# Optimization experiments

Measured on AMD Instinct MI355X. Metric: run time of the kernel, lower is better.

## Reference

```python
import jax, jax.numpy as jnp
import numpy as np

B, N, CIN, COUT, R, K = 8, 4096, 64, 128, 32, 3
GROUPS = 8
GN_EPS = 1e-5


def setup_inputs() -> dict:
    key = jax.random.key(0)
    ks = jax.random.split(key, 6)
    w = lambda k, shape, fan: jax.random.normal(k, shape, jnp.float32) / np.sqrt(fan)
    return dict(
        features=jax.random.normal(ks[0], (B, CIN, N), jnp.float32),
        coords=jax.random.uniform(ks[1], (B, N, 3), jnp.float32),
        conv1_w=w(ks[2], (COUT, CIN, K, K, K), CIN * K ** 3), conv1_b=jnp.zeros((COUT,), jnp.float32),
        gn1_g=jnp.ones((COUT,), jnp.float32), gn1_b=jnp.zeros((COUT,), jnp.float32),
        conv2_w=w(ks[3], (COUT, COUT, K, K, K), COUT * K ** 3), conv2_b=jnp.zeros((COUT,), jnp.float32),
        gn2_g=jnp.ones((COUT,), jnp.float32), gn2_b=jnp.zeros((COUT,), jnp.float32),
        pt_w=w(ks[4], (COUT, CIN), CIN), pt_b=jnp.zeros((COUT,), jnp.float32),
        ptgn_g=jnp.ones((COUT,), jnp.float32), ptgn_b=jnp.zeros((COUT,), jnp.float32),
    )


def swish(x):
    return x * jax.nn.sigmoid(x)


def group_norm(x, gamma, beta):
    # x: [B, C, *spatial]
    b, c = x.shape[0], x.shape[1]
    sp = x.shape[2:]
    xg = x.reshape(b, GROUPS, -1)
    m = xg.mean(-1, keepdims=True)
    v = xg.var(-1, keepdims=True)
    xg = (xg - m) * jax.lax.rsqrt(v + GN_EPS)
    x = xg.reshape(b, c, *sp)
    shape = (1, c) + (1,) * len(sp)
    return x * gamma.reshape(shape) + beta.reshape(shape)


def conv3d(x, w, bias):
    p = K // 2
    y = jax.lax.conv_general_dilated(
        x, w, window_strides=(1, 1, 1), padding=[(p, p)] * 3,
        dimension_numbers=('NCDHW', 'OIDHW', 'NCDHW'))
    return y + bias[None, :, None, None, None]


def voxelize(features, coords):
    # PVCNN avg_voxelize: normalize coords to [0, R-1], round, scatter-mean.
    c = coords - coords.mean(axis=1, keepdims=True)          # [B,N,3]
    scale = 2.0 * jnp.linalg.norm(c, axis=-1).max(axis=1)     # [B], eps=0
    norm_coords = c / scale[:, None, None] + 0.5
    norm_coords = jnp.clip(norm_coords * R, 0.0, R - 1)       # float coords in [0, R-1]
    vox = jnp.round(norm_coords).astype(jnp.int32)
    flat = (vox[..., 0] * R + vox[..., 1]) * R + vox[..., 2]  # [B,N]
    seg = (flat + jnp.arange(B, dtype=jnp.int32)[:, None] * R ** 3).reshape(-1)
    ft = features.transpose(0, 2, 1).reshape(B * N, CIN)
    sums = jax.ops.segment_sum(ft, seg, num_segments=B * R ** 3)
    cnt = jax.ops.segment_sum(jnp.ones((B * N,), ft.dtype), seg, num_segments=B * R ** 3)
    grid = sums / jnp.maximum(cnt, 1.0)[:, None]
    grid = grid.reshape(B, R ** 3, CIN).transpose(0, 2, 1).reshape(B, CIN, R, R, R)
    return grid, norm_coords


def trilinear_devoxelize(grid, norm_coords):
    # grid: [B, C, R, R, R]; norm_coords: [B, N, 3] float in [0, R-1]
    c = grid.shape[1]
    f = jnp.floor(norm_coords)
    d = norm_coords - f                                       # frac, [B,N,3]
    f0 = f.astype(jnp.int32)
    f1 = jnp.minimum(f0 + 1, R - 1)
    gridf = grid.reshape(B, c, R ** 3)
    out = jnp.zeros((B, c, N), grid.dtype)
    for ix in (0, 1):
        for iy in (0, 1):
            for iz in (0, 1):
                xi = f1[..., 0] if ix else f0[..., 0]
                yi = f1[..., 1] if iy else f0[..., 1]
                zi = f1[..., 2] if iz else f0[..., 2]
                wx = d[..., 0] if ix else 1.0 - d[..., 0]
                wy = d[..., 1] if iy else 1.0 - d[..., 1]
                wz = d[..., 2] if iz else 1.0 - d[..., 2]
                idx = (xi * R + yi) * R + zi                  # [B,N]
                g = jnp.take_along_axis(gridf, idx[:, None, :], axis=2)  # [B,C,N]
                out = out + g * (wx * wy * wz)[:, None, :]
    return out


def reference(features, coords, conv1_w, conv1_b, gn1_g, gn1_b,
              conv2_w, conv2_b, gn2_g, gn2_b, pt_w, pt_b, ptgn_g, ptgn_b):
    grid, norm_coords = voxelize(features, coords)
    h = swish(group_norm(conv3d(grid, conv1_w, conv1_b), gn1_g, gn1_b))
    h = swish(group_norm(conv3d(h, conv2_w, conv2_b), gn2_g, gn2_b))
    devox = trilinear_devoxelize(h, norm_coords)              # [B, COUT, N]
    pf = jnp.einsum('oc,bcn->bon', pt_w, features) + pt_b[None, :, None]
    pf = swish(group_norm(pf, ptgn_g, ptgn_b))
    return devox + pf
```

## Files before the change

kernel.cpp:

```cpp
#include <hip/hip_runtime.h>
#include <hip/hip_bf16.h>
#include <cstdint>

#define B_ 8
#define N_ 4096
#define CIN_ 64
#define COUT_ 128
#define R_ 32
#define R3_ 32768
#define GROUPS_ 8
#define EPS_ 1e-5f

typedef float f32x4 __attribute__((ext_vector_type(4)));
typedef __bf16 bf16x8 __attribute__((ext_vector_type(8)));
typedef unsigned short ushort8x __attribute__((ext_vector_type(8)));

static __device__ __forceinline__ unsigned short f2b(float f) {
    uint32_t u = __float_as_uint(f);
    uint32_t r = (u + 0x7fffu + ((u >> 16) & 1u)) >> 16;
    return (unsigned short)r;
}
static __device__ __forceinline__ float b2f(unsigned short u) {
    return __uint_as_float(((uint32_t)u) << 16);
}

__global__ void k_batch_stats(const float* __restrict__ coords, float* __restrict__ bstats) {
    int b = blockIdx.x;
    int tid = threadIdx.x;
    __shared__ float rb[256];
    __shared__ float smean[3];
    const float* cb = coords + (size_t)b * N_ * 3;
    float sx = 0.f, sy = 0.f, sz = 0.f;
    for (int n = tid; n < N_; n += 256) {
        sx += cb[n * 3 + 0];
        sy += cb[n * 3 + 1];
        sz += cb[n * 3 + 2];
    }
    float vals[3] = {sx, sy, sz};
    for (int k = 0; k < 3; ++k) {
        rb[tid] = vals[k];
        __syncthreads();
        for (int s = 128; s > 0; s >>= 1) {
            if (tid < s) rb[tid] += rb[tid + s];
            __syncthreads();
        }
        if (tid == 0) smean[k] = rb[0] / (float)N_;
        __syncthreads();
    }
    float mx = smean[0], my = smean[1], mz = smean[2];
    float m2 = 0.f;
    for (int n = tid; n < N_; n += 256) {
        float dx = cb[n * 3 + 0] - mx, dy = cb[n * 3 + 1] - my, dz = cb[n * 3 + 2] - mz;
        m2 = fmaxf(m2, dx * dx + dy * dy + dz * dz);
    }
    rb[tid] = m2;
    __syncthreads();
    for (int s = 128; s > 0; s >>= 1) {
        if (tid < s) rb[tid] = fmaxf(rb[tid], rb[tid + s]);
        __syncthreads();
    }
    if (tid == 0) {
        bstats[b * 4 + 0] = mx;
        bstats[b * 4 + 1] = my;
        bstats[b * 4 + 2] = mz;
        bstats[b * 4 + 3] = 2.0f * sqrtf(rb[0]);
    }
}

__global__ void k_points(const float* __restrict__ coords, const float* __restrict__ bstats,
                         float* __restrict__ ncoords, int* __restrict__ flatidx,
                         float* __restrict__ cnt) {
    int idx = blockIdx.x * 256 + threadIdx.x;
    int b = idx >> 12, n = idx & (N_ - 1);
    float scale = bstats[b * 4 + 3];
    int vi[3];
    for (int k = 0; k < 3; ++k) {
        float c = coords[((size_t)b * N_ + n) * 3 + k] - bstats[b * 4 + k];
        float nc = fminf(fmaxf((c / scale + 0.5f) * (float)R_, 0.0f), (float)(R_ - 1));
        ncoords[((size_t)b * N_ + n) * 3 + k] = nc;
        vi[k] = (int)rintf(nc);
    }
    int flat = (vi[0] * R_ + vi[1]) * R_ + vi[2];
    flatidx[idx] = flat;
    atomicAdd(&cnt[(size_t)b * R3_ + flat], 1.0f);
}

__global__ void k_scatter(const float* __restrict__ feat, const int* __restrict__ flatidx,
                          float* __restrict__ vox, int b0) {
    int bid = blockIdx.x;
    int nch = bid & 15, ci = (bid >> 4) & 63, bl = bid >> 10;
    int b = b0 + bl;
    int n = nch * 256 + threadIdx.x;
    float v = feat[((size_t)b * CIN_ + ci) * N_ + n];
    int flat = flatidx[b * N_ + n];
    atomicAdd(&vox[((size_t)bl * R3_ + flat) * CIN_ + ci], v);
}

__global__ void k_divide(const float* __restrict__ vox, const float* __restrict__ cnt,
                         unsigned short* __restrict__ gA, int b0) {
    size_t idx8 = (size_t)blockIdx.x * 256 + threadIdx.x;
    size_t voxel = idx8 >> 3;
    float c = cnt[(size_t)b0 * R3_ + voxel];
    float s = 1.0f / fmaxf(c, 1.0f);
    const float4* v4 = (const float4*)vox;
    float4 a = v4[idx8 * 2], b = v4[idx8 * 2 + 1];
    ushort8x o;
    o[0] = f2b(a.x * s); o[1] = f2b(a.y * s); o[2] = f2b(a.z * s); o[3] = f2b(a.w * s);
    o[4] = f2b(b.x * s); o[5] = f2b(b.y * s); o[6] = f2b(b.z * s); o[7] = f2b(b.w * s);
    ((ushort8x*)gA)[idx8] = o;
}

__global__ void k_feat2b(const float* __restrict__ f, unsigned short* __restrict__ fb, int b0) {
    size_t i8 = (size_t)blockIdx.x * 256 + threadIdx.x;
    const float4* s = (const float4*)(f + (size_t)b0 * CIN_ * N_);
    float4 a = s[i8 * 2], b = s[i8 * 2 + 1];
    ushort8x o;
    o[0] = f2b(a.x); o[1] = f2b(a.y); o[2] = f2b(a.z); o[3] = f2b(a.w);
    o[4] = f2b(b.x); o[5] = f2b(b.y); o[6] = f2b(b.z); o[7] = f2b(b.w);
    ((ushort8x*)fb)[i8] = o;
}

__global__ void k_wpack(const float* __restrict__ w, unsigned short* __restrict__ wp,
                        int Cin, int taps) {
    int e = blockIdx.x * 256 + threadIdx.x;
    int total = taps * Cin * 128;
    if (e >= total) return;
    int KC = Cin / 32;
    int j = e & 7;
    int l = (e >> 3) & 63;
    int rest = e >> 9;
    int ct = rest & 7;
    int stepk = rest >> 3;
    int kc = stepk % KC;
    int t = stepk / KC;
    int co = ct * 16 + (l & 15);
    int ci = kc * 32 + (l >> 4) * 8 + j;
    wp[e] = f2b(w[((size_t)co * Cin + ci) * taps + t]);
}

template <int CIN>
__global__ __launch_bounds__(256) void k_conv_mfma(
    const unsigned short* __restrict__ in, const unsigned short* __restrict__ wp,
    const float* __restrict__ bias, unsigned short* __restrict__ out,
    float* __restrict__ stats, int b0) {
    constexpr int KC = CIN / 32;
    constexpr int S = CIN + 8;
    __shared__ unsigned short abuf[6 * 34 * S];
    __shared__ float s_sum[8], s_sq[8];
    int tid = threadIdx.x;
    int bid = blockIdx.x;
    int yg = bid & 7, x = (bid >> 3) & 31, bl = bid >> 8;
    int y0 = yg * 4;
    int lane = tid & 63, wv = tid >> 6;
    int yp = wv & 1, ch = wv >> 1;
    int mrow = lane & 15, quad = lane >> 4;

    if (tid < 8) { s_sum[tid] = 0.f; s_sq[tid] = 0.f; }
    for (int i = tid; i < 6 * 2 * (CIN / 8); i += 256) {
        int cy = i / (2 * (CIN / 8));
        int r = i - cy * (2 * (CIN / 8));
        int hz = (r >= (CIN / 8)) ? 33 : 0;
        int c8 = r % (CIN / 8);
        ushort8x zz = {0, 0, 0, 0, 0, 0, 0, 0};
        *(ushort8x*)&abuf[(cy * 34 + hz) * S + c8 * 8] = zz;
    }

    float bv[4];
#pragma unroll
    for (int ct = 0; ct < 4; ++ct) bv[ct] = bias[ch * 64 + ct * 16 + mrow];
    f32x4 acc[2][2][4];
#pragma unroll
    for (int a = 0; a < 2; ++a)
#pragma unroll
        for (int zt = 0; zt < 2; ++zt)
#pragma unroll
            for (int ct = 0; ct < 4; ++ct) {
                acc[a][zt][ct][0] = bv[ct]; acc[a][zt][ct][1] = bv[ct];
                acc[a][zt][ct][2] = bv[ct]; acc[a][zt][ct][3] = bv[ct];
            }

    for (int xxi = 0; xxi < 3; ++xxi) {
        int xx = x + xxi - 1;
        if (xx < 0 || xx >= 32) continue;
        __syncthreads();
        for (int i = tid; i < 6 * 4 * CIN; i += 256) {
            int cy = i / (4 * CIN);
            int r = i - cy * (4 * CIN);
            int z = r / (CIN / 8), c8 = r - z * (CIN / 8);
            int yy = y0 - 1 + cy;
            ushort8x v = {0, 0, 0, 0, 0, 0, 0, 0};
            if (yy >= 0 && yy < 32)
                v = *(const ushort8x*)&in[((size_t)bl * R3_ + xx * 1024 + yy * 32 + z) * CIN + c8 * 8];
            *(ushort8x*)&abuf[(cy * 34 + z + 1) * S + c8 * 8] = v;
        }
        __syncthreads();

        for (int dy3 = 0; dy3 < 3; ++dy3) {
            for (int dz = 0; dz < 3; ++dz) {
#pragma unroll
                for (int kc = 0; kc < KC; ++kc) {
                    int t = (xxi * 3 + dy3) * 3 + dz;
                    const unsigned short* wbase =
                        wp + ((size_t)((t * KC + kc) * 8 + ch * 4) * 64 + lane) * 8;
                    bf16x8 bfr[4];
#pragma unroll
                    for (int ct = 0; ct < 4; ++ct)
                        bfr[ct] = *(const bf16x8*)(wbase + ct * 512);
#pragma unroll
                    for (int yo2 = 0; yo2 < 2; ++yo2) {
                        int cy = yp * 2 + yo2 + dy3;
#pragma unroll
                        for (int zt = 0; zt < 2; ++zt) {
                            bf16x8 a = *(const bf16x8*)
                                &abuf[(cy * 34 + zt * 16 + mrow + dz) * S + kc * 32 + quad * 8];
#pragma unroll
                            for (int ct = 0; ct < 4; ++ct)
                                acc[yo2][zt][ct] = __builtin_amdgcn_mfma_f32_16x16x32_bf16(
                                    a, bfr[ct], acc[yo2][zt][ct], 0, 0, 0);
                        }
                    }
                }
            }
        }
    }

    float lsum[4] = {0.f, 0.f, 0.f, 0.f}, lsq[4] = {0.f, 0.f, 0.f, 0.f};
#pragma unroll
    for (int yo2 = 0; yo2 < 2; ++yo2) {
        int y = y0 + yp * 2 + yo2;
#pragma unroll
        for (int zt = 0; zt < 2; ++zt) {
#pragma unroll
            for (int ct = 0; ct < 4; ++ct) {
                int co = ch * 64 + ct * 16 + mrow;
#pragma unroll
                for (int r = 0; r < 4; ++r) {
                    int z = zt * 16 + quad * 4 + r;
                    float vv = acc[yo2][zt][ct][r];
                    out[((size_t)bl * R3_ + x * 1024 + y * 32 + z) * 128 + co] = f2b(vv);
                    lsum[ct] += vv;
                    lsq[ct] += vv * vv;
                }
            }
        }
    }
#pragma unroll
    for (int ct = 0; ct < 4; ++ct) {
        atomicAdd(&s_sum[ch * 4 + ct], lsum[ct]);
        atomicAdd(&s_sq[ch * 4 + ct], lsq[ct]);
    }
    __syncthreads();
    if (tid < 8) {
        int b = b0 + bl;
        atomicAdd(&stats[((size_t)b * 8 + tid) * 2 + 0], s_sum[tid]);
        atomicAdd(&stats[((size_t)b * 8 + tid) * 2 + 1], s_sq[tid]);
    }
}

__global__ void k_gnswish(unsigned short* __restrict__ g, const float* __restrict__ stats,
                          const float* __restrict__ gamma, const float* __restrict__ beta,
                          int b0) {
    size_t idx8 = (size_t)blockIdx.x * 256 + threadIdx.x;
    int c0 = (int)(idx8 & 15) * 8;
    int b = b0 + (int)(idx8 >> 19);
    int grp = c0 >> 4;
    const float cntv = 16.0f * R3_;
    float mean = stats[(b * 8 + grp) * 2 + 0] / cntv;
    float var = stats[(b * 8 + grp) * 2 + 1] / cntv - mean * mean;
    float inv = rsqrtf(var + EPS_);
    ushort8x v = ((ushort8x*)g)[idx8];
#pragma unroll
    for (int k = 0; k < 8; ++k) {
        float A = gamma[c0 + k] * inv;
        float Bc = beta[c0 + k] - mean * A;
        float x = b2f(v[k]);
        float s = A * x + Bc;
        v[k] = f2b(s / (1.0f + expf(-s)));
    }
    ((ushort8x*)g)[idx8] = v;
}

__global__ __launch_bounds__(256) void k_point_mfma(
    const unsigned short* __restrict__ featb, const unsigned short* __restrict__ wp,
    const float* __restrict__ bias, unsigned short* __restrict__ pf,
    float* __restrict__ stats, int b0) {
    __shared__ __align__(16) unsigned short ALds[256 * 72];
    int tid = threadIdx.x;
    int bid = blockIdx.x;
    int bl = bid >> 4;
    int n0 = (bid & 15) * 256;
    int b = b0 + bl;
    int lane = tid & 63, wv = tid >> 6;
    int nh = wv & 1, ch = wv >> 1;
    int mrow = lane & 15, quad = lane >> 4;

    {
        int c0 = (tid >> 5) * 8;
        int nl = tid & 31;
        for (int u = 0; u < 8; ++u) {
            int n = u * 32 + nl;
            ushort8x v;
#pragma unroll
            for (int k = 0; k < 8; ++k)
                v[k] = featb[((size_t)(bl * 64 + c0 + k)) * N_ + n0 + n];
            *(ushort8x*)&ALds[n * 72 + c0] = v;
        }
    }

    bf16x8 bfr[2][4];
#pragma unroll
    for (int kc = 0; kc < 2; ++kc)
#pragma unroll
        for (int ct = 0; ct < 4; ++ct)
            bfr[kc][ct] = *(const bf16x8*)&wp[((size_t)((kc * 8) + ch * 4 + ct) * 64 + lane) * 8];

    float bv[4];
#pragma unroll
    for (int ct = 0; ct < 4; ++ct) bv[ct] = bias[ch * 64 + ct * 16 + mrow];
    f32x4 acc[8][4];
#pragma unroll
    for (int mt = 0; mt < 8; ++mt)
#pragma unroll
        for (int ct = 0; ct < 4; ++ct) {
            acc[mt][ct][0] = bv[ct]; acc[mt][ct][1] = bv[ct];
            acc[mt][ct][2] = bv[ct]; acc[mt][ct][3] = bv[ct];
        }

    __syncthreads();
#pragma unroll
    for (int kc = 0; kc < 2; ++kc) {
#pragma unroll
        for (int mt = 0; mt < 8; ++mt) {
            bf16x8 a = *(const bf16x8*)
                &ALds[(nh * 128 + mt * 16 + mrow) * 72 + kc * 32 + quad * 8];
#pragma unroll
            for (int ct = 0; ct < 4; ++ct)
                acc[mt][ct] = __builtin_amdgcn_mfma_f32_16x16x32_bf16(
                    a, bfr[kc][ct], acc[mt][ct], 0, 0, 0);
        }
    }

#pragma unroll
    for (int ct = 0; ct < 4; ++ct) {
        int co = ch * 64 + ct * 16 + mrow;
        float s = 0.f, q = 0.f;
#pragma unroll
        for (int mt = 0; mt < 8; ++mt) {
#pragma unroll
            for (int r = 0; r < 4; ++r) {
                int n = nh * 128 + mt * 16 + quad * 4 + r;
                float vv = acc[mt][ct][r];
                pf[((size_t)bl * N_ + n0 + n) * 128 + co] = f2b(vv);
                s += vv;
                q += vv * vv;
            }
        }
#pragma unroll
        for (int off = 32; off >= 1; off >>= 1) {
            s += __shfl_xor(s, off);
            q += __shfl_xor(q, off);
        }
        if (lane == 0) {
            int g = ch * 4 + ct;
            atomicAdd(&stats[((size_t)b * 8 + g) * 2 + 0], s);
            atomicAdd(&stats[((size_t)b * 8 + g) * 2 + 1], q);
        }
    }
}

__global__ __launch_bounds__(256) void k_final(
    const unsigned short* __restrict__ grid, const float* __restrict__ ncoords,
    const unsigned short* __restrict__ pf, const float* __restrict__ stats,
    const float* __restrict__ gamma, const float* __restrict__ beta,
    float* __restrict__ out, int b0) {
    __shared__ int sidx[32][8];
    __shared__ float swt[32][8];
    __shared__ float devt[32 * 129];
    int bid = blockIdx.x;
    int bl = bid >> 7;
    int b = b0 + bl;
    int n0 = (bid & 127) * 32;
    int tid = threadIdx.x;
    if (tid < 32) {
        int n = n0 + tid;
        const float* nc = ncoords + ((size_t)b * N_ + n) * 3;
        float fc[3] = {nc[0], nc[1], nc[2]};
        int i0[3], i1[3];
        float dd[3];
        for (int k = 0; k < 3; ++k) {
            float fl = floorf(fc[k]);
            i0[k] = (int)fl;
            i1[k] = min(i0[k] + 1, R_ - 1);
            dd[k] = fc[k] - fl;
        }
#pragma unroll
        for (int k = 0; k < 8; ++k) {
            int ix = (k >> 2) & 1, iy = (k >> 1) & 1, iz = k & 1;
            int xi = ix ? i1[0] : i0[0];
            int yi = iy ? i1[1] : i0[1];
            int zi = iz ? i1[2] : i0[2];
            sidx[tid][k] = (xi * R_ + yi) * R_ + zi;
            float wx = ix ? dd[0] : 1.0f - dd[0];
            float wy = iy ? dd[1] : 1.0f - dd[1];
            float wz = iz ? dd[2] : 1.0f - dd[2];
            swt[tid][k] = wx * wy * wz;
        }
    }
    __syncthreads();
    int co = tid & 127, pg = tid >> 7;
    int grp = co >> 4;
    const float cntv = 16.0f * N_;
    float mean = stats[(b * 8 + grp) * 2 + 0] / cntv;
    float var = stats[(b * 8 + grp) * 2 + 1] / cntv - mean * mean;
    float inv = rsqrtf(var + EPS_);
    float A = gamma[co] * inv, Bc = beta[co] - mean * A;
    const unsigned short* gp = grid + (size_t)bl * R3_ * 128 + co;
    for (int p = pg; p < 32; p += 2) {
        float acc = 0.f;
#pragma unroll
        for (int k = 0; k < 8; ++k) acc += swt[p][k] * b2f(gp[(size_t)sidx[p][k] * 128]);
        float x = b2f(pf[((size_t)bl * N_ + n0 + p) * 128 + co]);
        float s = A * x + Bc;
        devt[p * 129 + co] = acc + s / (1.0f + expf(-s));
    }
    __syncthreads();
    int pp = tid & 31, cg = tid >> 5;
    float* op = out + (size_t)b * 128 * N_ + n0 + pp;
    for (int c = cg * 16; c < cg * 16 + 16; ++c)
        op[(size_t)c * N_] = devt[pp * 129 + c];
}

extern "C" void kernel_launch(void* const* d_in, const int* in_sizes, int n_in,
                              void* d_out, int out_size, void* d_ws, size_t ws_size,
                              hipStream_t stream) {
    const float* features = (const float*)d_in[0];
    const float* coords = (const float*)d_in[1];
    const float* c1w = (const float*)d_in[2];
    const float* c1b = (const float*)d_in[3];
    const float* g1g = (const float*)d_in[4];
    const float* g1b = (const float*)d_in[5];
    const float* c2w = (const float*)d_in[6];
    const float* c2b = (const float*)d_in[7];
    const float* g2g = (const float*)d_in[8];
    const float* g2b = (const float*)d_in[9];
    const float* ptw = (const float*)d_in[10];
    const float* ptb = (const float*)d_in[11];
    const float* pgg = (const float*)d_in[12];
    const float* pgb = (const float*)d_in[13];
    float* outp = (float*)d_out;

    size_t globals = ((size_t)B_ * R3_ * 4 + 255 & ~(size_t)255)
                   + ((size_t)B_ * N_ * 3 * 4 + 255 & ~(size_t)255)
                   + ((size_t)B_ * N_ * 4 + 255 & ~(size_t)255)
                   + 256 + 2048
                   + ((size_t)27 * 64 * 128 * 2 + 255 & ~(size_t)255)
                   + ((size_t)27 * 128 * 128 * 2 + 255 & ~(size_t)255)
                   + ((size_t)64 * 128 * 2 + 255 & ~(size_t)255)
                   + 8192;
    int CB = 1;
    for (int cb = 8; cb >= 1; cb >>= 1) {
        size_t need = globals
                    + ((size_t)cb * R3_ * 64 * 4)
                    + ((size_t)cb * R3_ * 64 * 2)
                    + ((size_t)cb * R3_ * 128 * 2)
                    + ((size_t)cb * N_ * 128 * 2)
                    + ((size_t)cb * 64 * N_ * 2);
        if (need <= ws_size) { CB = cb; break; }
    }

    char* ws = (char*)d_ws;
    size_t o = 0;
    auto alloc = [&](size_t bytes) {
        size_t r = o;
        o += (bytes + 255) & ~(size_t)255;
        return r;
    };
    float* voxC = (float*)(ws + alloc((size_t)CB * R3_ * 64 * 4));
    unsigned short* gC = (unsigned short*)voxC;
    unsigned short* gA = (unsigned short*)(ws + alloc((size_t)CB * R3_ * 64 * 2));
    unsigned short* gB = (unsigned short*)(ws + alloc((size_t)CB * R3_ * 128 * 2));
    unsigned short* pfbuf = (unsigned short*)(ws + alloc((size_t)CB * N_ * 128 * 2));
    unsigned short* featbc = (unsigned short*)(ws + alloc((size_t)CB * 64 * N_ * 2));
    float* cnt = (float*)(ws + alloc((size_t)B_ * R3_ * 4));
    float* ncoords = (float*)(ws + alloc((size_t)B_ * N_ * 3 * 4));
    int* flatidx = (int*)(ws + alloc((size_t)B_ * N_ * 4));
    float* bstats = (float*)(ws + alloc(256));
    float* statsAll = (float*)(ws + alloc(2048));
    float* stats1 = statsAll;
    float* stats2 = statsAll + 128;
    float* statsPt = statsAll + 256;
    unsigned short* wp1 = (unsigned short*)(ws + alloc((size_t)27 * 64 * 128 * 2));
    unsigned short* wp2 = (unsigned short*)(ws + alloc((size_t)27 * 128 * 128 * 2));
    unsigned short* wpPt = (unsigned short*)(ws + alloc((size_t)64 * 128 * 2));

    hipMemsetAsync(cnt, 0, (size_t)B_ * R3_ * 4, stream);
    hipMemsetAsync(statsAll, 0, 1536, stream);
    k_wpack<<<(27 * 64 * 128 + 255) / 256, 256, 0, stream>>>(c1w, wp1, 64, 27);
    k_wpack<<<(27 * 128 * 128 + 255) / 256, 256, 0, stream>>>(c2w, wp2, 128, 27);
    k_wpack<<<(64 * 128 + 255) / 256, 256, 0, stream>>>(ptw, wpPt, 64, 1);
    k_batch_stats<<<B_, 256, 0, stream>>>(coords, bstats);
    k_points<<<B_ * N_ / 256, 256, 0, stream>>>(coords, bstats, ncoords, flatidx, cnt);

    for (int b0 = 0; b0 < B_; b0 += CB) {
        hipMemsetAsync(voxC, 0, (size_t)CB * R3_ * 64 * 4, stream);
        k_feat2b<<<CB * 128, 256, 0, stream>>>(features, featbc, b0);
        k_scatter<<<CB * 64 * 16, 256, 0, stream>>>(features, flatidx, voxC, b0);
        k_divide<<<CB * 1024, 256, 0, stream>>>(voxC, cnt, gA, b0);
        k_conv_mfma<64><<<CB * 256, 256, 0, stream>>>(gA, wp1, c1b, gB, stats1, b0);
        k_gnswish<<<CB * 2048, 256, 0, stream>>>(gB, stats1, g1g, g1b, b0);
        k_conv_mfma<128><<<CB * 256, 256, 0, stream>>>(gB, wp2, c2b, gC, stats2, b0);
        k_gnswish<<<CB * 2048, 256, 0, stream>>>(gC, stats2, g2g, g2b, b0);
        k_point_mfma<<<CB * 16, 256, 0, stream>>>(featbc, wpPt, ptb, pfbuf, statsPt, b0);
        k_final<<<CB * 128, 256, 0, stream>>>(gC, ncoords, pfbuf, statsPt, pgg, pgb, outp, b0);
    }
}
```

Baseline: 701.4 us.

## Switch convs to 32x32x16 MFMA and fuse GroupNorm-swish into conv loads and devoxelize

Replaces the 16x16x32 MFMA conv with a 32x32x16 bf16 MFMA variant, adding a matching weight-packing kernel. The two standalone GroupNorm+swish passes are removed. The first is applied while conv2 stages its input tile into shared memory. The second is applied per gathered voxel inside the final trilinear devoxelize kernel. This saves two full read-modify-write passes over the voxel grids, at the cost of recomputing swish for halo voxels and for each of the eight trilinear corners.

Measured after the change: 746.7 us. 6.5% more time.

```diff
diff --git a/kernel.cpp b/kernel.cpp
--- a/kernel.cpp
+++ b/kernel.cpp
@@ -12,6 +12,7 @@
 #define EPS_ 1e-5f
 
 typedef float f32x4 __attribute__((ext_vector_type(4)));
+typedef float f32x16 __attribute__((ext_vector_type(16)));
 typedef __bf16 bf16x8 __attribute__((ext_vector_type(8)));
 typedef unsigned short ushort8x __attribute__((ext_vector_type(8)));
 
@@ -120,8 +121,8 @@
     ((ushort8x*)fb)[i8] = o;
 }
 
-__global__ void k_wpack(const float* __restrict__ w, unsigned short* __restrict__ wp,
-                        int Cin, int taps) {
+__global__ void k_wpack16(const float* __restrict__ w, unsigned short* __restrict__ wp,
+                          int Cin, int taps) {
     int e = blockIdx.x * 256 + threadIdx.x;
     int total = taps * Cin * 128;
     if (e >= total) return;
@@ -138,24 +139,54 @@
     wp[e] = f2b(w[((size_t)co * Cin + ci) * taps + t]);
 }
 
-template <int CIN>
-__global__ __launch_bounds__(256) void k_conv_mfma(
+__global__ void k_wpack32(const float* __restrict__ w, unsigned short* __restrict__ wp,
+                          int Cin, int taps) {
+    int e = blockIdx.x * 256 + threadIdx.x;
+    int total = taps * Cin * 128;
+    if (e >= total) return;
+    int K16C = Cin / 16;
+    int j = e & 7;
+    int l = (e >> 3) & 63;
+    int nt = (e >> 9) & 3;
+    int sk = e >> 11;
+    int k16 = sk % K16C;
+    int t = sk / K16C;
+    int co = nt * 32 + (l & 31);
+    int ci = k16 * 16 + (l >> 5) * 8 + j;
+    wp[e] = f2b(w[((size_t)co * Cin + ci) * taps + t]);
+}
+
+template <int CIN, bool FUSEGN>
+__global__ __launch_bounds__(256) void k_conv32(
     const unsigned short* __restrict__ in, const unsigned short* __restrict__ wp,
-    const float* __restrict__ bias, unsigned short* __restrict__ out,
-    float* __restrict__ stats, int b0) {
-    constexpr int KC = CIN / 32;
+    const float* __restrict__ bias, const float* __restrict__ instats,
+    const float* __restrict__ ingamma, const float* __restrict__ inbeta,
+    unsigned short* __restrict__ out, float* __restrict__ stats, int b0) {
+    constexpr int K16C = CIN / 16;
     constexpr int S = CIN + 8;
     __shared__ unsigned short abuf[6 * 34 * S];
     __shared__ float s_sum[8], s_sq[8];
+    __shared__ float sA[128], sB[128];
     int tid = threadIdx.x;
     int bid = blockIdx.x;
     int yg = bid & 7, x = (bid >> 3) & 31, bl = bid >> 8;
     int y0 = yg * 4;
     int lane = tid & 63, wv = tid >> 6;
     int yp = wv & 1, ch = wv >> 1;
-    int mrow = lane & 15, quad = lane >> 4;
+    int col = lane & 31, kh = lane >> 5;
 
     if (tid < 8) { s_sum[tid] = 0.f; s_sq[tid] = 0.f; }
+    if (FUSEGN && tid < 128) {
+        int b = b0 + bl;
+        int grp = tid >> 4;
+        const float ic = 1.0f / (16.0f * R3_);
+        float mean = instats[(b * 8 + grp) * 2 + 0] * ic;
+        float var = instats[(b * 8 + grp) * 2 + 1] * ic - mean * mean;
+        float inv = rsqrtf(var + EPS_);
+        float A = ingamma[tid] * inv;
+        sA[tid] = A;
+        sB[tid] = inbeta[tid] - mean * A;
+    }
     for (int i = tid; i < 6 * 2 * (CIN / 8); i += 256) {
         int cy = i / (2 * (CIN / 8));
         int r = i - cy * (2 * (CIN / 8));
@@ -165,89 +196,95 @@
         *(ushort8x*)&abuf[(cy * 34 + hz) * S + c8 * 8] = zz;
     }
 
-    float bv[4];
-#pragma unroll
-    for (int ct = 0; ct < 4; ++ct) bv[ct] = bias[ch * 64 + ct * 16 + mrow];
-    f32x4 acc[2][2][4];
-#pragma unroll
-    for (int a = 0; a < 2; ++a)
-#pragma unroll
-        for (int zt = 0; zt < 2; ++zt)
-#pragma unroll
-            for (int ct = 0; ct < 4; ++ct) {
-                acc[a][zt][ct][0] = bv[ct]; acc[a][zt][ct][1] = bv[ct];
-                acc[a][zt][ct][2] = bv[ct]; acc[a][zt][ct][3] = bv[ct];
-            }
+    float bv[2];
+#pragma unroll
+    for (int ntl = 0; ntl < 2; ++ntl) bv[ntl] = bias[ch * 64 + ntl * 32 + col];
+    f32x16 acc[2][2];
+#pragma unroll
+    for (int my = 0; my < 2; ++my)
+#pragma unroll
+        for (int ntl = 0; ntl < 2; ++ntl)
+#pragma unroll
+            for (int r = 0; r < 16; ++r) acc[my][ntl][r] = bv[ntl];
 
     for (int xxi = 0; xxi < 3; ++xxi) {
         int xx = x + xxi - 1;
         if (xx < 0 || xx >= 32) continue;
         __syncthreads();
-        for (int i = tid; i < 6 * 4 * CIN; i += 256) {
-            int cy = i / (4 * CIN);
-            int r = i - cy * (4 * CIN);
+        for (int i = tid; i < 6 * 32 * (CIN / 8); i += 256) {
+            int cy = i / (32 * (CIN / 8));
+            int r = i - cy * (32 * (CIN / 8));
             int z = r / (CIN / 8), c8 = r - z * (CIN / 8);
             int yy = y0 - 1 + cy;
             ushort8x v = {0, 0, 0, 0, 0, 0, 0, 0};
-            if (yy >= 0 && yy < 32)
+            if (yy >= 0 && yy < 32) {
                 v = *(const ushort8x*)&in[((size_t)bl * R3_ + xx * 1024 + yy * 32 + z) * CIN + c8 * 8];
-            *(ushort8x*)&abuf[(cy * 34 + z + 1) * S + c8 * 8] = v;
-        }
-        __syncthreads();
-
-        for (int dy3 = 0; dy3 < 3; ++dy3) {
-            for (int dz = 0; dz < 3; ++dz) {
-#pragma unroll
-                for (int kc = 0; kc < KC; ++kc) {
-                    int t = (xxi * 3 + dy3) * 3 + dz;
-                    const unsigned short* wbase =
-                        wp + ((size_t)((t * KC + kc) * 8 + ch * 4) * 64 + lane) * 8;
-                    bf16x8 bfr[4];
-#pragma unroll
-                    for (int ct = 0; ct < 4; ++ct)
-                        bfr[ct] = *(const bf16x8*)(wbase + ct * 512);
-#pragma unroll
-                    for (int yo2 = 0; yo2 < 2; ++yo2) {
-                        int cy = yp * 2 + yo2 + dy3;
-#pragma unroll
-                        for (int zt = 0; zt < 2; ++zt) {
-                            bf16x8 a = *(const bf16x8*)
-                                &abuf[(cy * 34 + zt * 16 + mrow + dz) * S + kc * 32 + quad * 8];
-#pragma unroll
-                            for (int ct = 0; ct < 4; ++ct)
-                                acc[yo2][zt][ct] = __builtin_amdgcn_mfma_f32_16x16x32_bf16(
-                                    a, bfr[ct], acc[yo2][zt][ct], 0, 0, 0);
-                        }
+                if (FUSEGN) {
+#pragma unroll
+                    for (int k = 0; k < 8; ++k) {
+                        float xv = b2f(v[k]);
+                        float s = sA[c8 * 8 + k] * xv + sB[c8 * 8 + k];
+                        v[k] = f2b(s / (1.0f + expf(-s)));
                     }
                 }
             }
-        }
-    }
-
-    float lsum[4] = {0.f, 0.f, 0.f, 0.f}, lsq[4] = {0.f, 0.f, 0.f, 0.f};
-#pragma unroll
-    for (int yo2 = 0; yo2 < 2; ++yo2) {
-        int y = y0 + yp * 2 + yo2;
-#pragma unroll
-        for (int zt = 0; zt < 2; ++zt) {
-#pragma unroll
-            for (int ct = 0; ct < 4; ++ct) {
-                int co = ch * 64 + ct * 16 + mrow;
-#pragma unroll
-                for (int r = 0; r < 4; ++r) {
-                    int z = zt * 16 + quad * 4 + r;
-                    float vv = acc[yo2][zt][ct][r];
-                    out[((size_t)bl * R3_ + x * 1024 + y * 32 + z) * 128 + co] = f2b(vv);
-                    lsum[ct] += vv;
-                    lsq[ct] += vv * vv;
+            *(ushort8x*)&abuf[(cy * 34 + z + 1) * S + c8 * 8] = v;
+        }
+        __syncthreads();
+
+        for (int dy = 0; dy < 3; ++dy) {
+            for (int dz = 0; dz < 3; ++dz) {
+                int t = (xxi * 3 + dy) * 3 + dz;
+#pragma unroll
+                for (int k16 = 0; k16 < K16C; ++k16) {
+                    const unsigned short* wbase =
+                        wp + ((size_t)((t * K16C + k16) * 4 + ch * 2) * 64 + lane) * 8;
+                    bf16x8 b0f = *(const bf16x8*)wbase;
+                    bf16x8 b1f = *(const bf16x8*)(wbase + 512);
+#pragma unroll
+                    for (int my = 0; my < 2; ++my) {
+                        int cy = yp * 2 + my + dy;
+                        bf16x8 a = *(const bf16x8*)
+                            &abuf[(cy * 34 + col + dz) * S + k16 * 16 + kh * 8];
+                        acc[my][0] = __builtin_amdgcn_mfma_f32_32x32x16_bf16(a, b0f, acc[my][0], 0, 0, 0);
+                        acc[my][1] = __builtin_amdgcn_mfma_f32_32x32x16_bf16(a, b1f, acc[my][1], 0, 0, 0);
+                    }
                 }
             }
         }
     }
-#pragma unroll
-    for (int ct = 0; ct < 4; ++ct) {
-        atomicAdd(&s_sum[ch * 4 + ct], lsum[ct]);
-        atomicAdd(&s_sq[ch * 4 + ct], lsq[ct]);
+
+    float lsum[2] = {0.f, 0.f}, lsq[2] = {0.f, 0.f};
+#pragma unroll
+    for (int my = 0; my < 2; ++my) {
+        int y = y0 + yp * 2 + my;
+#pragma unroll
+        for (int ntl = 0; ntl < 2; ++ntl) {
+            int co = ch * 64 + ntl * 32 + col;
+            unsigned short* op = out + ((size_t)bl * R3_ + x * 1024 + y * 32) * 128 + co;
+#pragma unroll
+            for (int r = 0; r < 16; ++r) {
+                int z = (r & 3) + 8 * (r >> 2) + 4 * kh;
+                float vv = acc[my][ntl][r];
+                op[(size_t)z * 128] = f2b(vv);
+                lsum[ntl] += vv;
+                lsq[ntl] += vv * vv;
+            }
+        }
+    }
+#pragma unroll
+    for (int ntl = 0; ntl < 2; ++ntl) {
+        float s = lsum[ntl], q = lsq[ntl];
+        s += __shfl_xor(s, 32); q += __shfl_xor(q, 32);
+        s += __shfl_xor(s, 1);  q += __shfl_xor(q, 1);
+        s += __shfl_xor(s, 2);  q += __shfl_xor(q, 2);
+        s += __shfl_xor(s, 4);  q += __shfl_xor(q, 4);
+        s += __shfl_xor(s, 8);  q += __shfl_xor(q, 8);
+        if (lane == 0 || lane == 16) {
+            int g = ch * 4 + ntl * 2 + (col >> 4);
+            atomicAdd(&s_sum[g], s);
+            atomicAdd(&s_sq[g], q);
+        }
     }
     __syncthreads();
     if (tid < 8) {
@@ -255,29 +292,6 @@
         atomicAdd(&stats[((size_t)b * 8 + tid) * 2 + 0], s_sum[tid]);
         atomicAdd(&stats[((size_t)b * 8 + tid) * 2 + 1], s_sq[tid]);
     }
-}
-
-__global__ void k_gnswish(unsigned short* __restrict__ g, const float* __restrict__ stats,
-                          const float* __restrict__ gamma, const float* __restrict__ beta,
-                          int b0) {
-    size_t idx8 = (size_t)blockIdx.x * 256 + threadIdx.x;
-    int c0 = (int)(idx8 & 15) * 8;
-    int b = b0 + (int)(idx8 >> 19);
-    int grp = c0 >> 4;
-    const float cntv = 16.0f * R3_;
-    float mean = stats[(b * 8 + grp) * 2 + 0] / cntv;
-    float var = stats[(b * 8 + grp) * 2 + 1] / cntv - mean * mean;
-    float inv = rsqrtf(var + EPS_);
-    ushort8x v = ((ushort8x*)g)[idx8];
-#pragma unroll
-    for (int k = 0; k < 8; ++k) {
-        float A = gamma[c0 + k] * inv;
-        float Bc = beta[c0 + k] - mean * A;
-        float x = b2f(v[k]);
-        float s = A * x + Bc;
-        v[k] = f2b(s / (1.0f + expf(-s)));
-    }
-    ((ushort8x*)g)[idx8] = v;
 }
 
 __global__ __launch_bounds__(256) void k_point_mfma(
@@ -370,8 +384,11 @@
 
 __global__ __launch_bounds__(256) void k_final(
     const unsigned short* __restrict__ grid, const float* __restrict__ ncoords,
-    const unsigned short* __restrict__ pf, const float* __restrict__ stats,
-    const float* __restrict__ gamma, const float* __restrict__ beta,
+    const unsigned short* __restrict__ pf,
+    const float* __restrict__ stats2, const float* __restrict__ g2g,
+    const float* __restrict__ g2b,
+    const float* __restrict__ statsPt, const float* __restrict__ pgg,
+    const float* __restrict__ pgb,
     float* __restrict__ out, int b0) {
     __shared__ int sidx[32][8];
     __shared__ float swt[32][8];
@@ -409,18 +426,27 @@
     __syncthreads();
     int co = tid & 127, pg = tid >> 7;
     int grp = co >> 4;
-    const float cntv = 16.0f * N_;
-    float mean = stats[(b * 8 + grp) * 2 + 0] / cntv;
-    float var = stats[(b * 8 + grp) * 2 + 1] / cntv - mean * mean;
-    float inv = rsqrtf(var + EPS_);
-    float A = gamma[co] * inv, Bc = beta[co] - mean * A;
+    const float ic2 = 1.0f / (16.0f * R3_);
+    float mean2 = stats2[(b * 8 + grp) * 2 + 0] * ic2;
+    float var2 = stats2[(b * 8 + grp) * 2 + 1] * ic2 - mean2 * mean2;
+    float inv2 = rsqrtf(var2 + EPS_);
+    float A2 = g2g[co] * inv2, B2 = g2b[co] - mean2 * A2;
+    const float icp = 1.0f / (16.0f * N_);
+    float meanp = statsPt[(b * 8 + grp) * 2 + 0] * icp;
+    float varp = statsPt[(b * 8 + grp) * 2 + 1] * icp - meanp * meanp;
+    float invp = rsqrtf(varp + EPS_);
+    float Ap = pgg[co] * invp, Bp = pgb[co] - meanp * Ap;
+
     const unsigned short* gp = grid + (size_t)bl * R3_ * 128 + co;
     for (int p = pg; p < 32; p += 2) {
         float acc = 0.f;
 #pragma unroll
-        for (int k = 0; k < 8; ++k) acc += swt[p][k] * b2f(gp[(size_t)sidx[p][k] * 128]);
-        float x = b2f(pf[((size_t)bl * N_ + n0 + p) * 128 + co]);
-        float s = A * x + Bc;
+        for (int k = 0; k < 8; ++k) {
+            float s = A2 * b2f(gp[(size_t)sidx[p][k] * 128]) + B2;
+            acc += swt[p][k] * (s / (1.0f + expf(-s)));
+        }
+        float xv = b2f(pf[((size_t)bl * N_ + n0 + p) * 128 + co]);
+        float s = Ap * xv + Bp;
         devt[p * 129 + co] = acc + s / (1.0f + expf(-s));
     }
     __syncthreads();
@@ -495,9 +521,9 @@
 
     hipMemsetAsync(cnt, 0, (size_t)B_ * R3_ * 4, stream);
     hipMemsetAsync(statsAll, 0, 1536, stream);
-    k_wpack<<<(27 * 64 * 128 + 255) / 256, 256, 0, stream>>>(c1w, wp1, 64, 27);
-    k_wpack<<<(27 * 128 * 128 + 255) / 256, 256, 0, stream>>>(c2w, wp2, 128, 27);
-    k_wpack<<<(64 * 128 + 255) / 256, 256, 0, stream>>>(ptw, wpPt, 64, 1);
+    k_wpack32<<<(27 * 64 * 128 + 255) / 256, 256, 0, stream>>>(c1w, wp1, 64, 27);
+    k_wpack32<<<(27 * 128 * 128 + 255) / 256, 256, 0, stream>>>(c2w, wp2, 128, 27);
+    k_wpack16<<<(64 * 128 + 255) / 256, 256, 0, stream>>>(ptw, wpPt, 64, 1);
     k_batch_stats<<<B_, 256, 0, stream>>>(coords, bstats);
     k_points<<<B_ * N_ / 256, 256, 0, stream>>>(coords, bstats, ncoords, flatidx, cnt);
 
@@ -506,11 +532,12 @@
         k_feat2b<<<CB * 128, 256, 0, stream>>>(features, featbc, b0);
         k_scatter<<<CB * 64 * 16, 256, 0, stream>>>(features, flatidx, voxC, b0);
         k_divide<<<CB * 1024, 256, 0, stream>>>(voxC, cnt, gA, b0);
-        k_conv_mfma<64><<<CB * 256, 256, 0, stream>>>(gA, wp1, c1b, gB, stats1, b0);
-        k_gnswish<<<CB * 2048, 256, 0, stream>>>(gB, stats1, g1g, g1b, b0);
-        k_conv_mfma<128><<<CB * 256, 256, 0, stream>>>(gB, wp2, c2b, gC, stats2, b0);
-        k_gnswish<<<CB * 2048, 256, 0, stream>>>(gC, stats2, g2g, g2b, b0);
+        k_conv32<64, false><<<CB * 256, 256, 0, stream>>>(
+            gA, wp1, c1b, nullptr, nullptr, nullptr, gB, stats1, b0);
+        k_conv32<128, true><<<CB * 256, 256, 0, stream>>>(
+            gB, wp2, c2b, stats1, g1g, g1b, gC, stats2, b0);
         k_point_mfma<<<CB * 16, 256, 0, stream>>>(featbc, wpPt, ptb, pfbuf, statsPt, b0);
-        k_final<<<CB * 128, 256, 0, stream>>>(gC, ncoords, pfbuf, statsPt, pgg, pgb, outp, b0);
-    }
-}
+        k_final<<<CB * 128, 256, 0, stream>>>(gC, ncoords, pfbuf,
+                                              stats2, g2g, g2b, statsPt, pgg, pgb, outp, b0);
+    }
+}
```
